# Kernel optimization log

Hardware: AMD Instinct MI355X
Metric: run time of the kernel (lower is better)

Reference implementation:

```python
import jax, jax.numpy as jnp
import numpy as np

NOISE_EPS = 0.01
TOP_K = 2


def setup_inputs() -> dict:
    key = jax.random.key(0)
    k1, k2, k3, k4 = jax.random.split(key, 4)
    B, S, D, E = 4, 4096, 2048, 64
    x = jax.random.normal(k1, (B, S, D), dtype=jnp.float32)
    raw_noise = jax.random.normal(k2, (B, S, E), dtype=jnp.float32)
    # gating_mlp: single Linear(D -> E), init std=0.02, zero bias
    W_gate = 0.02 * jax.random.normal(k3, (E, D), dtype=jnp.float32)
    b_gate = jnp.zeros((E,), dtype=jnp.float32)
    # noise_projection: Linear(D -> E, bias=False), init std=1/sqrt(D)
    W_noise = (1.0 / np.sqrt(D)) * jax.random.normal(k4, (E, D), dtype=jnp.float32)
    return {"x": x, "raw_noise": raw_noise, "W_gate": W_gate, "b_gate": b_gate, "W_noise": W_noise}


def reference(x, raw_noise, W_gate, b_gate, W_noise):
    # gate logits: [B,S,E]
    logits = jnp.einsum("bsd,ed->bse", x, W_gate) + b_gate
    # noisy top-k routing (training path)
    noise_stddev = jax.nn.softplus(jnp.einsum("bsd,ed->bse", x, W_noise)) + NOISE_EPS
    noisy = logits + raw_noise * noise_stddev
    top_v, top_i = jax.lax.top_k(noisy, TOP_K)            # [B,S,K]
    top_p = jax.nn.softmax(top_v.astype(jnp.float32), axis=-1).astype(noisy.dtype)
    B, S, E = noisy.shape
    T = B * S
    flat_logits = noisy.reshape(T, E)
    flat_i = top_i.reshape(T, TOP_K)
    flat_p = top_p.reshape(T, TOP_K)
    sparse = jnp.zeros((T, E), dtype=noisy.dtype).at[jnp.arange(T)[:, None], flat_i].set(flat_p)
    # aux load-balancing loss
    indicator = (sparse > 0.0).astype(jnp.float32)
    fraction_routed = indicator.sum(axis=0) / T           # f_e
    router_probs = jax.nn.softmax(flat_logits.astype(jnp.float32), axis=-1)
    avg_prob = router_probs.mean(axis=0)                  # p_e
    aux_loss = jnp.sum(fraction_routed * avg_prob) * E
    return sparse.reshape(B, S, E), aux_loss.astype(noisy.dtype)
```

## Files before the change

kernel.cpp:

```cpp
#include <hip/hip_runtime.h>
#include <math.h>

#define TOK 16384
#define DD  2048
#define EE  64
#define MT  32
#define BK  32
#define NKC 32
#define LDA 40

typedef _Float16 half4v __attribute__((ext_vector_type(4)));
typedef _Float16 half8  __attribute__((ext_vector_type(8)));
typedef float    floatx4 __attribute__((ext_vector_type(4)));

__global__ void build_wf(const float* __restrict__ Wg, const float* __restrict__ Wn,
                         _Float16* __restrict__ wf) {
  int tid  = blockIdx.x * 256 + threadIdx.x;
  int lane = tid & 63;
  int kc   = (tid >> 6) & 63;
  int ct   = tid >> 12;
  int col  = (ct & 3) * 16 + (lane & 15);
  int k    = kc * 32 + (lane >> 4) * 8;
  const float* W = (ct < 4) ? Wg : Wn;
  const float* src = W + (size_t)col * DD + k;
  float4 a = *reinterpret_cast<const float4*>(src);
  float4 b = *reinterpret_cast<const float4*>(src + 4);
  float v[8] = {a.x, a.y, a.z, a.w, b.x, b.y, b.z, b.w};
  half8 hi, lo;
#pragma unroll
  for (int j = 0; j < 8; ++j) {
    _Float16 h = (_Float16)v[j];
    hi[j] = h;
    lo[j] = (_Float16)(v[j] - (float)h);
  }
  size_t base = (((size_t)(ct * 64 + kc) * 2 + 0) * 64 + lane) * 8;
  *reinterpret_cast<half8*>(wf + base)       = hi;
  *reinterpret_cast<half8*>(wf + base + 512) = lo;
}

__global__ __launch_bounds__(512, 4)
void gating_kernel(const float* __restrict__ x, const float* __restrict__ rn,
                   const _Float16* __restrict__ wf, const float* __restrict__ bg,
                   float* __restrict__ out,
                   float* __restrict__ cnt_g, float* __restrict__ psum_g) {
  __shared__ char smem[33920];
  _Float16* xs   = (_Float16*)smem;
  float*    Pacc = (float*)smem;
  float*    Vb   = (float*)(smem + 16384);
  float*    Eb   = (float*)(smem + 24832);
  float*    isum = (float*)(smem + 33280);
  int*      ti   = (int*)(smem + 33408);
  float*    tp   = (float*)(smem + 33664);

  const int t  = threadIdx.x;
  const int g  = t >> 8;
  const int tg = t & 255;
  const int w4 = tg >> 6;
  const int l  = t & 63;
  const int q  = l >> 4;
  const int cl = l & 15;
  const int c  = w4 * 16 + cl;
  const int t0 = blockIdx.x * MT;

  const int stok = tg >> 3;
  const int skof = (tg & 7) * 4;
  const float* xrow = x + (size_t)(t0 + stok) * DD + g * (NKC * BK) + skof;

  float bgv = 0.f;
  float rnv[2][4] = {{0.f,0.f,0.f,0.f},{0.f,0.f,0.f,0.f}};
  if (g == 0) {
    bgv = bg[c];
#pragma unroll
    for (int mt = 0; mt < 2; ++mt)
#pragma unroll
      for (int r = 0; r < 4; ++r)
        rnv[mt][r] = rn[(size_t)(t0 + mt * 16 + q * 4 + r) * EE + c];
  }

  floatx4 acc[2][2];
#pragma unroll
  for (int mt = 0; mt < 2; ++mt)
#pragma unroll
    for (int nt = 0; nt < 2; ++nt) acc[mt][nt] = (floatx4)0.f;

  const half8* wfp = (const half8*)wf;
  half8 B[2][2][2];

  {
    float4 a = *reinterpret_cast<const float4*>(xrow);
    float v[4] = {a.x, a.y, a.z, a.w};
    half4v hi, lo;
#pragma unroll
    for (int j = 0; j < 4; ++j) {
      _Float16 h = (_Float16)v[j];
      hi[j] = h;
      lo[j] = (_Float16)(v[j] - (float)h);
    }
    *reinterpret_cast<half4v*>(&xs[((g * 2 + 0) * 2 + 0) * (MT * LDA) + stok * LDA + skof]) = hi;
    *reinterpret_cast<half4v*>(&xs[((g * 2 + 0) * 2 + 1) * (MT * LDA) + stok * LDA + skof]) = lo;
#pragma unroll
    for (int nt = 0; nt < 2; ++nt) {
      const int ct = w4 + nt * 4;
#pragma unroll
      for (int s = 0; s < 2; ++s)
        B[0][nt][s] = wfp[((size_t)(ct * 64 + g * NKC) * 2 + s) * 64 + l];
    }
  }

#pragma unroll 4
  for (int kc = 0; kc < NKC; ++kc) {
    const int cur = kc & 1;
    const bool more = (kc < NKC - 1);
    float4 pa;
    if (more) {
      pa = *reinterpret_cast<const float4*>(xrow + (kc + 1) * BK);
#pragma unroll
      for (int nt = 0; nt < 2; ++nt) {
        const int ct = w4 + nt * 4;
#pragma unroll
        for (int s = 0; s < 2; ++s)
          B[cur ^ 1][nt][s] = wfp[((size_t)(ct * 64 + g * NKC + kc + 1) * 2 + s) * 64 + l];
      }
    }
    __syncthreads();

    half8 Ah[2], Al[2];
#pragma unroll
    for (int mt = 0; mt < 2; ++mt) {
      Ah[mt] = *reinterpret_cast<const half8*>(
          &xs[((g * 2 + cur) * 2 + 0) * (MT * LDA) + (mt * 16 + cl) * LDA + q * 8]);
      Al[mt] = *reinterpret_cast<const half8*>(
          &xs[((g * 2 + cur) * 2 + 1) * (MT * LDA) + (mt * 16 + cl) * LDA + q * 8]);
    }
#pragma unroll
    for (int mt = 0; mt < 2; ++mt)
#pragma unroll
      for (int nt = 0; nt < 2; ++nt)
        acc[mt][nt] = __builtin_amdgcn_mfma_f32_16x16x32_f16(Ah[mt], B[cur][nt][0], acc[mt][nt], 0, 0, 0);
#pragma unroll
    for (int mt = 0; mt < 2; ++mt)
#pragma unroll
      for (int nt = 0; nt < 2; ++nt)
        acc[mt][nt] = __builtin_amdgcn_mfma_f32_16x16x32_f16(Ah[mt], B[cur][nt][1], acc[mt][nt], 0, 0, 0);
#pragma unroll
    for (int mt = 0; mt < 2; ++mt)
#pragma unroll
      for (int nt = 0; nt < 2; ++nt)
        acc[mt][nt] = __builtin_amdgcn_mfma_f32_16x16x32_f16(Al[mt], B[cur][nt][0], acc[mt][nt], 0, 0, 0);

    if (more) {
      float v[4] = {pa.x, pa.y, pa.z, pa.w};
      half4v hi, lo;
#pragma unroll
      for (int j = 0; j < 4; ++j) {
        _Float16 h = (_Float16)v[j];
        hi[j] = h;
        lo[j] = (_Float16)(v[j] - (float)h);
      }
      *reinterpret_cast<half4v*>(&xs[((g * 2 + (cur ^ 1)) * 2 + 0) * (MT * LDA) + stok * LDA + skof]) = hi;
      *reinterpret_cast<half4v*>(&xs[((g * 2 + (cur ^ 1)) * 2 + 1) * (MT * LDA) + stok * LDA + skof]) = lo;
    }
  }

  __syncthreads();

  if (g == 1) {
#pragma unroll
    for (int mt = 0; mt < 2; ++mt)
#pragma unroll
      for (int nt = 0; nt < 2; ++nt)
#pragma unroll
        for (int r = 0; r < 4; ++r)
          Pacc[((((w4 * 2 + mt) * 2 + nt) * 4) + r) * 64 + l] = acc[mt][nt][r];
  }
  __syncthreads();

  if (g == 0) {
#pragma unroll
    for (int mt = 0; mt < 2; ++mt)
#pragma unroll
      for (int nt = 0; nt < 2; ++nt)
#pragma unroll
        for (int r = 0; r < 4; ++r)
          acc[mt][nt][r] += Pacc[((((w4 * 2 + mt) * 2 + nt) * 4) + r) * 64 + l];

#pragma unroll
    for (int mt = 0; mt < 2; ++mt)
#pragma unroll
      for (int r = 0; r < 4; ++r) {
        const int tk = mt * 16 + q * 4 + r;
        float gt = acc[mt][0][r] + bgv;
        float h  = acc[mt][1][r];
        float sp = (h > 20.f) ? h : log1pf(expf(h));
        float v  = gt + rnv[mt][r] * (sp + 0.01f);
        Vb[tk * 66 + c] = v;
        Eb[tk * 66 + c] = expf(v);
      }
  }
  __syncthreads();

  if (t < MT) {
    float v1 = -1e30f, v2 = -1e30f;
    int   i1 = 0, i2 = 0;
    float s = 0.f;
    for (int e = 0; e < EE; ++e) {
      float v = Vb[t * 66 + e];
      s += Eb[t * 66 + e];
      if (v > v1)      { v2 = v1; i2 = i1; v1 = v; i1 = e; }
      else if (v > v2) { v2 = v;  i2 = e; }
    }
    isum[t] = 1.f / s;
    ti[t * 2 + 0] = i1; ti[t * 2 + 1] = i2;
    float e2 = expf(v2 - v1);
    float dn = 1.f + e2;
    tp[t * 2 + 0] = 1.f / dn;
    tp[t * 2 + 1] = e2 / dn;
  }
  __syncthreads();

  {
    const int m  = t >> 4;
    const int c0 = (t & 15) * 4;
    const int i1 = ti[m * 2 + 0], i2 = ti[m * 2 + 1];
    const float p1 = tp[m * 2 + 0], p2 = tp[m * 2 + 1];
    float o[4];
#pragma unroll
    for (int j = 0; j < 4; ++j) {
      const int col = c0 + j;
      o[j] = (col == i1) ? p1 : ((col == i2) ? p2 : 0.f);
    }
    *reinterpret_cast<float4*>(out + (size_t)(t0 + m) * EE + c0) =
        make_float4(o[0], o[1], o[2], o[3]);
  }

  if (t < EE) {
    float s = 0.f;
    int   cn = 0;
#pragma unroll
    for (int m = 0; m < MT; ++m) {
      s  += Eb[m * 66 + t] * isum[m];
      cn += (ti[m * 2 + 0] == t) + (ti[m * 2 + 1] == t);
    }
    atomicAdd(&psum_g[t], s);
    atomicAdd(&cnt_g[t], (float)cn);
  }
}

__global__ void aux_kernel(const float* __restrict__ cnt_g,
                           const float* __restrict__ psum_g,
                           float* __restrict__ out) {
  int e = threadIdx.x;
  float v = cnt_g[e] * psum_g[e];
#pragma unroll
  for (int o = 32; o > 0; o >>= 1) v += __shfl_down(v, o);
  if (e == 0)
    out[(size_t)TOK * EE] = v * ((float)EE / ((float)TOK * (float)TOK));
}

extern "C" void kernel_launch(void* const* d_in, const int* in_sizes, int n_in,
                              void* d_out, int out_size, void* d_ws, size_t ws_size,
                              hipStream_t stream) {
  const float* x  = (const float*)d_in[0];
  const float* rn = (const float*)d_in[1];
  const float* Wg = (const float*)d_in[2];
  const float* bg = (const float*)d_in[3];
  const float* Wn = (const float*)d_in[4];
  float* out    = (float*)d_out;
  float* cnt_g  = (float*)d_ws;
  float* psum_g = cnt_g + EE;
  _Float16* wf  = (_Float16*)((float*)d_ws + 128);

  hipMemsetAsync(d_ws, 0, 2 * EE * sizeof(float), stream);
  build_wf<<<128, 256, 0, stream>>>(Wg, Wn, wf);
  gating_kernel<<<TOK / MT, 512, 0, stream>>>(x, rn, wf, bg, out, cnt_g, psum_g);
  aux_kernel<<<1, 64, 0, stream>>>(cnt_g, psum_g, out);
}
```

Before: 235.1 us.

## Load x directly into registers and give each wave all 64 output columns

The gating GEMM is restructured so each block has 2 waves instead of 8. Each wave splits K in half and computes all 64 columns for 32 tokens, reading x straight from global memory into MFMA A fragments. This removes the LDS staging of x and the per-step __syncthreads. The weight buffer is re-laid out k-chunk-major so one wave loads 16 B fragments per step, and x loads are prefetched two steps ahead. The cost is far fewer threads per block, higher register pressure (launch_bounds 128,1) and lower occupancy, relying on ILP to hide memory latency.

```diff
diff --git a/kernel.cpp b/kernel.cpp
--- a/kernel.cpp
+++ b/kernel.cpp
@@ -5,11 +5,8 @@
 #define DD  2048
 #define EE  64
 #define MT  32
-#define BK  32
-#define NKC 32
-#define LDA 40
-
-typedef _Float16 half4v __attribute__((ext_vector_type(4)));
+#define KCW 32
+
 typedef _Float16 half8  __attribute__((ext_vector_type(8)));
 typedef float    floatx4 __attribute__((ext_vector_type(4)));
 
@@ -33,169 +30,144 @@
     hi[j] = h;
     lo[j] = (_Float16)(v[j] - (float)h);
   }
-  size_t base = (((size_t)(ct * 64 + kc) * 2 + 0) * 64 + lane) * 8;
+  size_t base = (((size_t)(kc * 8 + ct) * 2 + 0) * 64 + lane) * 8;
   *reinterpret_cast<half8*>(wf + base)       = hi;
   *reinterpret_cast<half8*>(wf + base + 512) = lo;
 }
 
-__global__ __launch_bounds__(512, 4)
+#define KBODY(kc, CUR, NXT)                                                        \
+  {                                                                                \
+    half8 Ah[2], Al[2];                                                            \
+    _Pragma("unroll")                                                              \
+    for (int mt = 0; mt < 2; ++mt) {                                               \
+      float v[8] = {Aa[CUR][mt].x, Aa[CUR][mt].y, Aa[CUR][mt].z, Aa[CUR][mt].w,    \
+                    Ab[CUR][mt].x, Ab[CUR][mt].y, Ab[CUR][mt].z, Ab[CUR][mt].w};   \
+      _Pragma("unroll")                                                            \
+      for (int j = 0; j < 8; ++j) {                                                \
+        _Float16 h = (_Float16)v[j];                                               \
+        Ah[mt][j] = h;                                                             \
+        Al[mt][j] = (_Float16)(v[j] - (float)h);                                   \
+      }                                                                            \
+    }                                                                              \
+    if ((kc) + 2 < KCW) {                                                          \
+      _Pragma("unroll")                                                            \
+      for (int mt = 0; mt < 2; ++mt) {                                             \
+        Aa[CUR][mt] = *reinterpret_cast<const float4*>(xp[mt] + ((kc) + 2) * 32);  \
+        Ab[CUR][mt] = *reinterpret_cast<const float4*>(xp[mt] + ((kc) + 2) * 32 + 4); \
+      }                                                                            \
+    }                                                                              \
+    if ((kc) + 1 < KCW) {                                                          \
+      _Pragma("unroll")                                                            \
+      for (int f = 0; f < 16; ++f) Bf[NXT][f] = wp[((kc) + 1) * 1024 + f * 64];    \
+    }                                                                              \
+    _Pragma("unroll")                                                              \
+    for (int mt = 0; mt < 2; ++mt)                                                 \
+      _Pragma("unroll")                                                            \
+      for (int ct = 0; ct < 8; ++ct)                                               \
+        acc[mt][ct] = __builtin_amdgcn_mfma_f32_16x16x32_f16(                      \
+            Ah[mt], Bf[CUR][ct * 2 + 0], acc[mt][ct], 0, 0, 0);                    \
+    _Pragma("unroll")                                                              \
+    for (int mt = 0; mt < 2; ++mt)                                                 \
+      _Pragma("unroll")                                                            \
+      for (int ct = 0; ct < 8; ++ct)                                               \
+        acc[mt][ct] = __builtin_amdgcn_mfma_f32_16x16x32_f16(                      \
+            Ah[mt], Bf[CUR][ct * 2 + 1], acc[mt][ct], 0, 0, 0);                    \
+    _Pragma("unroll")                                                              \
+    for (int mt = 0; mt < 2; ++mt)                                                 \
+      _Pragma("unroll")                                                            \
+      for (int ct = 0; ct < 8; ++ct)                                               \
+        acc[mt][ct] = __builtin_amdgcn_mfma_f32_16x16x32_f16(                      \
+            Al[mt], Bf[CUR][ct * 2 + 0], acc[mt][ct], 0, 0, 0);                    \
+  }
+
+__global__ __launch_bounds__(128, 1)
 void gating_kernel(const float* __restrict__ x, const float* __restrict__ rn,
                    const _Float16* __restrict__ wf, const float* __restrict__ bg,
                    float* __restrict__ out,
                    float* __restrict__ cnt_g, float* __restrict__ psum_g) {
-  __shared__ char smem[33920];
-  _Float16* xs   = (_Float16*)smem;
-  float*    Pacc = (float*)smem;
-  float*    Vb   = (float*)(smem + 16384);
-  float*    Eb   = (float*)(smem + 24832);
-  float*    isum = (float*)(smem + 33280);
-  int*      ti   = (int*)(smem + 33408);
-  float*    tp   = (float*)(smem + 33664);
+  __shared__ float Pacc[64 * 64];
+  __shared__ float Vb[MT * 65];
+  __shared__ float Eb[MT * 65];
+  __shared__ float isum[MT];
+  __shared__ int   ti[MT * 2];
+  __shared__ float tp[MT * 2];
 
   const int t  = threadIdx.x;
-  const int g  = t >> 8;
-  const int tg = t & 255;
-  const int w4 = tg >> 6;
+  const int w  = t >> 6;
   const int l  = t & 63;
   const int q  = l >> 4;
   const int cl = l & 15;
-  const int c  = w4 * 16 + cl;
   const int t0 = blockIdx.x * MT;
 
-  const int stok = tg >> 3;
-  const int skof = (tg & 7) * 4;
-  const float* xrow = x + (size_t)(t0 + stok) * DD + g * (NKC * BK) + skof;
-
-  float bgv = 0.f;
-  float rnv[2][4] = {{0.f,0.f,0.f,0.f},{0.f,0.f,0.f,0.f}};
-  if (g == 0) {
-    bgv = bg[c];
+  const float* xp[2];
+  xp[0] = x + (size_t)(t0 + cl) * DD + w * (KCW * 32) + q * 8;
+  xp[1] = xp[0] + (size_t)16 * DD;
+
+  const half8* wp = reinterpret_cast<const half8*>(wf) + (size_t)(w * KCW) * 16 * 64 + l;
+
+  floatx4 acc[2][8];
+#pragma unroll
+  for (int mt = 0; mt < 2; ++mt)
+#pragma unroll
+    for (int ct = 0; ct < 8; ++ct) acc[mt][ct] = (floatx4)0.f;
+
+  float4 Aa[2][2], Ab[2][2];
+  half8  Bf[2][16];
+
+#pragma unroll
+  for (int mt = 0; mt < 2; ++mt) {
+    Aa[0][mt] = *reinterpret_cast<const float4*>(xp[mt]);
+    Ab[0][mt] = *reinterpret_cast<const float4*>(xp[mt] + 4);
+    Aa[1][mt] = *reinterpret_cast<const float4*>(xp[mt] + 32);
+    Ab[1][mt] = *reinterpret_cast<const float4*>(xp[mt] + 36);
+  }
+#pragma unroll
+  for (int f = 0; f < 16; ++f) Bf[0][f] = wp[f * 64];
+
+  for (int kc2 = 0; kc2 < KCW; kc2 += 2) {
+    KBODY(kc2, 0, 1)
+    KBODY(kc2 + 1, 1, 0)
+  }
+
+  if (w == 1) {
 #pragma unroll
     for (int mt = 0; mt < 2; ++mt)
 #pragma unroll
-      for (int r = 0; r < 4; ++r)
-        rnv[mt][r] = rn[(size_t)(t0 + mt * 16 + q * 4 + r) * EE + c];
-  }
-
-  floatx4 acc[2][2];
-#pragma unroll
-  for (int mt = 0; mt < 2; ++mt)
-#pragma unroll
-    for (int nt = 0; nt < 2; ++nt) acc[mt][nt] = (floatx4)0.f;
-
-  const half8* wfp = (const half8*)wf;
-  half8 B[2][2][2];
-
-  {
-    float4 a = *reinterpret_cast<const float4*>(xrow);
-    float v[4] = {a.x, a.y, a.z, a.w};
-    half4v hi, lo;
-#pragma unroll
-    for (int j = 0; j < 4; ++j) {
-      _Float16 h = (_Float16)v[j];
-      hi[j] = h;
-      lo[j] = (_Float16)(v[j] - (float)h);
-    }
-    *reinterpret_cast<half4v*>(&xs[((g * 2 + 0) * 2 + 0) * (MT * LDA) + stok * LDA + skof]) = hi;
-    *reinterpret_cast<half4v*>(&xs[((g * 2 + 0) * 2 + 1) * (MT * LDA) + stok * LDA + skof]) = lo;
-#pragma unroll
-    for (int nt = 0; nt < 2; ++nt) {
-      const int ct = w4 + nt * 4;
-#pragma unroll
-      for (int s = 0; s < 2; ++s)
-        B[0][nt][s] = wfp[((size_t)(ct * 64 + g * NKC) * 2 + s) * 64 + l];
-    }
-  }
-
-#pragma unroll 4
-  for (int kc = 0; kc < NKC; ++kc) {
-    const int cur = kc & 1;
-    const bool more = (kc < NKC - 1);
-    float4 pa;
-    if (more) {
-      pa = *reinterpret_cast<const float4*>(xrow + (kc + 1) * BK);
-#pragma unroll
-      for (int nt = 0; nt < 2; ++nt) {
-        const int ct = w4 + nt * 4;
-#pragma unroll
-        for (int s = 0; s < 2; ++s)
-          B[cur ^ 1][nt][s] = wfp[((size_t)(ct * 64 + g * NKC + kc + 1) * 2 + s) * 64 + l];
-      }
-    }
-    __syncthreads();
-
-    half8 Ah[2], Al[2];
-#pragma unroll
-    for (int mt = 0; mt < 2; ++mt) {
-      Ah[mt] = *reinterpret_cast<const half8*>(
-          &xs[((g * 2 + cur) * 2 + 0) * (MT * LDA) + (mt * 16 + cl) * LDA + q * 8]);
-      Al[mt] = *reinterpret_cast<const half8*>(
-          &xs[((g * 2 + cur) * 2 + 1) * (MT * LDA) + (mt * 16 + cl) * LDA + q * 8]);
-    }
+      for (int ct = 0; ct < 8; ++ct)
+#pragma unroll
+        for (int r = 0; r < 4; ++r)
+          Pacc[((mt * 8 + ct) * 4 + r) * 64 + l] = acc[mt][ct][r];
+  }
+  __syncthreads();
+
+  if (w == 0) {
 #pragma unroll
     for (int mt = 0; mt < 2; ++mt)
 #pragma unroll
-      for (int nt = 0; nt < 2; ++nt)
-        acc[mt][nt] = __builtin_amdgcn_mfma_f32_16x16x32_f16(Ah[mt], B[cur][nt][0], acc[mt][nt], 0, 0, 0);
+      for (int ct = 0; ct < 8; ++ct)
+#pragma unroll
+        for (int r = 0; r < 4; ++r)
+          acc[mt][ct][r] += Pacc[((mt * 8 + ct) * 4 + r) * 64 + l];
+
+    float bgv[4];
+#pragma unroll
+    for (int ct = 0; ct < 4; ++ct) bgv[ct] = bg[ct * 16 + cl];
+
 #pragma unroll
     for (int mt = 0; mt < 2; ++mt)
 #pragma unroll
-      for (int nt = 0; nt < 2; ++nt)
-        acc[mt][nt] = __builtin_amdgcn_mfma_f32_16x16x32_f16(Ah[mt], B[cur][nt][1], acc[mt][nt], 0, 0, 0);
-#pragma unroll
-    for (int mt = 0; mt < 2; ++mt)
-#pragma unroll
-      for (int nt = 0; nt < 2; ++nt)
-        acc[mt][nt] = __builtin_amdgcn_mfma_f32_16x16x32_f16(Al[mt], B[cur][nt][0], acc[mt][nt], 0, 0, 0);
-
-    if (more) {
-      float v[4] = {pa.x, pa.y, pa.z, pa.w};
-      half4v hi, lo;
-#pragma unroll
-      for (int j = 0; j < 4; ++j) {
-        _Float16 h = (_Float16)v[j];
-        hi[j] = h;
-        lo[j] = (_Float16)(v[j] - (float)h);
-      }
-      *reinterpret_cast<half4v*>(&xs[((g * 2 + (cur ^ 1)) * 2 + 0) * (MT * LDA) + stok * LDA + skof]) = hi;
-      *reinterpret_cast<half4v*>(&xs[((g * 2 + (cur ^ 1)) * 2 + 1) * (MT * LDA) + stok * LDA + skof]) = lo;
-    }
-  }
-
-  __syncthreads();
-
-  if (g == 1) {
-#pragma unroll
-    for (int mt = 0; mt < 2; ++mt)
-#pragma unroll
-      for (int nt = 0; nt < 2; ++nt)
-#pragma unroll
-        for (int r = 0; r < 4; ++r)
-          Pacc[((((w4 * 2 + mt) * 2 + nt) * 4) + r) * 64 + l] = acc[mt][nt][r];
-  }
-  __syncthreads();
-
-  if (g == 0) {
-#pragma unroll
-    for (int mt = 0; mt < 2; ++mt)
-#pragma unroll
-      for (int nt = 0; nt < 2; ++nt)
-#pragma unroll
-        for (int r = 0; r < 4; ++r)
-          acc[mt][nt][r] += Pacc[((((w4 * 2 + mt) * 2 + nt) * 4) + r) * 64 + l];
-
-#pragma unroll
-    for (int mt = 0; mt < 2; ++mt)
-#pragma unroll
-      for (int r = 0; r < 4; ++r) {
-        const int tk = mt * 16 + q * 4 + r;
-        float gt = acc[mt][0][r] + bgv;
-        float h  = acc[mt][1][r];
-        float sp = (h > 20.f) ? h : log1pf(expf(h));
-        float v  = gt + rnv[mt][r] * (sp + 0.01f);
-        Vb[tk * 66 + c] = v;
-        Eb[tk * 66 + c] = expf(v);
-      }
+      for (int ct = 0; ct < 4; ++ct)
+#pragma unroll
+        for (int r = 0; r < 4; ++r) {
+          const int tk = mt * 16 + q * 4 + r;
+          const int c  = ct * 16 + cl;
+          float gt = acc[mt][ct][r] + bgv[ct];
+          float h  = acc[mt][ct + 4][r];
+          float sp = (h > 20.f) ? h : log1pf(expf(h));
+          float v  = gt + rn[(size_t)(t0 + tk) * EE + c] * (sp + 0.01f);
+          Vb[tk * 65 + c] = v;
+          Eb[tk * 65 + c] = expf(v);
+        }
   }
   __syncthreads();
 
@@ -204,8 +176,8 @@
     int   i1 = 0, i2 = 0;
     float s = 0.f;
     for (int e = 0; e < EE; ++e) {
-      float v = Vb[t * 66 + e];
-      s += Eb[t * 66 + e];
+      float v = Vb[t * 65 + e];
+      s += Eb[t * 65 + e];
       if (v > v1)      { v2 = v1; i2 = i1; v1 = v; i1 = e; }
       else if (v > v2) { v2 = v;  i2 = e; }
     }
@@ -218,9 +190,11 @@
   }
   __syncthreads();
 
-  {
-    const int m  = t >> 4;
-    const int c0 = (t & 15) * 4;
+#pragma unroll
+  for (int i = 0; i < 4; ++i) {
+    const int idx = t + i * 128;
+    const int m   = idx >> 4;
+    const int c0  = (idx & 15) * 4;
     const int i1 = ti[m * 2 + 0], i2 = ti[m * 2 + 1];
     const float p1 = tp[m * 2 + 0], p2 = tp[m * 2 + 1];
     float o[4];
@@ -238,7 +212,7 @@
     int   cn = 0;
 #pragma unroll
     for (int m = 0; m < MT; ++m) {
-      s  += Eb[m * 66 + t] * isum[m];
+      s  += Eb[m * 65 + t] * isum[m];
       cn += (ti[m * 2 + 0] == t) + (ti[m * 2 + 1] == t);
     }
     atomicAdd(&psum_g[t], s);
@@ -272,6 +246,6 @@
 
   hipMemsetAsync(d_ws, 0, 2 * EE * sizeof(float), stream);
   build_wf<<<128, 256, 0, stream>>>(Wg, Wn, wf);
-  gating_kernel<<<TOK / MT, 512, 0, stream>>>(x, rn, wf, bg, out, cnt_g, psum_g);
+  gating_kernel<<<TOK / MT, 128, 0, stream>>>(x, rn, wf, bg, out, cnt_g, psum_g);
   aux_kernel<<<1, 64, 0, stream>>>(cnt_g, psum_g, out);
 }
```

Result: slower. 259.8 us (+10.5%).
